# Kernel optimization log

Hardware: AMD Instinct MI355X
Metric: run time of the kernel (lower is better)

## Reference

```python
import jax, jax.numpy as jnp
import numpy as np

N_NODES = 50000
N_EDGES = 500000
NODE_DIM = 128
EDGE_DIM = 128
HIDDEN = 256


def setup_inputs() -> dict:
    key = jax.random.key(0)
    k1, k2, k3, k4, k5 = jax.random.split(key, 5)
    node_features = jax.random.normal(k1, (N_NODES, NODE_DIM), dtype=jnp.float32)
    edge_features = jax.random.normal(k2, (N_EDGES, EDGE_DIM), dtype=jnp.float32)
    edge_index = jax.random.randint(k3, (2, N_EDGES), 0, N_NODES, dtype=jnp.int64)
    in_dim = 2 * NODE_DIM + EDGE_DIM
    W1 = jax.random.normal(k4, (in_dim, HIDDEN), dtype=jnp.float32) * (1.0 / np.sqrt(in_dim))
    b1 = jnp.zeros((HIDDEN,), dtype=jnp.float32)
    W2 = jax.random.normal(k5, (HIDDEN, EDGE_DIM), dtype=jnp.float32) * (1.0 / np.sqrt(HIDDEN))
    b2 = jnp.zeros((EDGE_DIM,), dtype=jnp.float32)
    return {"node_features": node_features, "edge_features": edge_features,
            "edge_index": edge_index, "W1": W1, "b1": b1, "W2": W2, "b2": b2}


def reference(node_features, edge_features, edge_index, W1, b1, W2, b2):
    # h_edge' = h_edge + MLP(concat(h_src, h_dst, h_edge)); dropout is identity (eval)
    src, dst = edge_index[0], edge_index[1]
    h_src = node_features[src]                    # (E, node_dim)
    h_dst = node_features[dst]                    # (E, node_dim)
    combined = jnp.concatenate([h_src, h_dst, edge_features], axis=1)  # (E, 2*nd+ed)
    h = jax.nn.relu(combined @ W1 + b1)           # (E, hidden)
    update = h @ W2 + b2                          # (E, edge_dim)
    return edge_features + update
```

## Files before the change

kernel.cpp:

```cpp
#include <hip/hip_runtime.h>

#define E_TOTAL   500000
#define NN        50000
#define ND        128
#define ED        128
#define HID       256
#define IND       384
#define EB        64
#define NBLOCKS   ((E_TOTAL + EB - 1) / EB)

typedef float  f32x4  __attribute__((ext_vector_type(4)));
typedef short  bf16x8 __attribute__((ext_vector_type(8)));

__device__ __forceinline__ unsigned short f2bf(float f) {
    unsigned int u = __float_as_uint(f);
    u += 0x7FFFu + ((u >> 16) & 1u);
    return (unsigned short)(u >> 16);
}
__device__ __forceinline__ float bf2f(unsigned short h) {
    return __uint_as_float(((unsigned int)h) << 16);
}

__global__ void prep_w1(const float* __restrict__ w1, unsigned short* __restrict__ w1t) {
    int i = blockIdx.x * blockDim.x + threadIdx.x;
    if (i >= IND * HID) return;
    int k = i / HID, n = i % HID;
    w1t[n * IND + k] = f2bf(w1[i]);
}

__global__ void prep_w2(const float* __restrict__ w2, unsigned short* __restrict__ w2t) {
    int i = blockIdx.x * blockDim.x + threadIdx.x;
    if (i >= HID * ED) return;
    int k = i / ED, n = i % ED;
    w2t[n * HID + k] = f2bf(w2[i]);
}

__global__ __launch_bounds__(256, 2)
void prep_ptab(const float* __restrict__ nf,
               const unsigned short* __restrict__ w1t,
               const float* __restrict__ b1,
               unsigned short* __restrict__ Psrc,
               unsigned short* __restrict__ Pdst) {
    __shared__ unsigned short An[EB * ND];
    const int tid  = threadIdx.x;
    const int base = blockIdx.x * EB;
    const int lane = tid & 63;
    const int w    = tid >> 6;
    const int l15  = lane & 15;
    const int lhi  = lane >> 4;

    #pragma unroll
    for (int it = 0; it < 4; ++it) {
        int item = tid + it * 256;
        int row = item >> 4, cc = item & 15;
        int nidx = base + row;
        if (nidx >= NN) nidx = NN - 1;
        const float* p = nf + (size_t)nidx * ND + cc * 8;
        float4 f0 = *(const float4*)p;
        float4 f1 = *(const float4*)(p + 4);
        bf16x8 val;
        val[0] = (short)f2bf(f0.x); val[1] = (short)f2bf(f0.y);
        val[2] = (short)f2bf(f0.z); val[3] = (short)f2bf(f0.w);
        val[4] = (short)f2bf(f1.x); val[5] = (short)f2bf(f1.y);
        val[6] = (short)f2bf(f1.z); val[7] = (short)f2bf(f1.w);
        *(bf16x8*)(An + row * ND + ((cc * 8) ^ ((row & 7) * 8))) = val;
    }
    __syncthreads();

    f32x4 accs[4][4], accd[4][4];
    #pragma unroll
    for (int mt = 0; mt < 4; ++mt)
        #pragma unroll
        for (int nt = 0; nt < 4; ++nt) { accs[mt][nt] = (f32x4)0.0f; accd[mt][nt] = (f32x4)0.0f; }

    #pragma unroll
    for (int ks = 0; ks < 4; ++ks) {
        int c0 = ks * 32 + lhi * 8;
        bf16x8 a[4];
        #pragma unroll
        for (int mt = 0; mt < 4; ++mt) {
            int row = mt * 16 + l15;
            a[mt] = *(const bf16x8*)(An + row * ND + (c0 ^ ((row & 7) * 8)));
        }
        #pragma unroll
        for (int nt = 0; nt < 4; ++nt) {
            int n = w * 64 + nt * 16 + l15;
            bf16x8 bs = *(const bf16x8*)(w1t + (size_t)n * IND + c0);
            bf16x8 bd = *(const bf16x8*)(w1t + (size_t)n * IND + 128 + c0);
            #pragma unroll
            for (int mt = 0; mt < 4; ++mt) {
                accs[mt][nt] = __builtin_amdgcn_mfma_f32_16x16x32_bf16(a[mt], bs, accs[mt][nt], 0, 0, 0);
                accd[mt][nt] = __builtin_amdgcn_mfma_f32_16x16x32_bf16(a[mt], bd, accd[mt][nt], 0, 0, 0);
            }
        }
    }

    #pragma unroll
    for (int nt = 0; nt < 4; ++nt) {
        int col = w * 64 + nt * 16 + l15;
        float bias = b1[col];
        #pragma unroll
        for (int mt = 0; mt < 4; ++mt) {
            #pragma unroll
            for (int r = 0; r < 4; ++r) {
                int row = mt * 16 + lhi * 4 + r;
                int nidx = base + row;
                if (nidx < NN) {
                    size_t off = (size_t)nidx * HID + col;
                    Psrc[off] = f2bf(accs[mt][nt][r] + bias);
                    Pdst[off] = f2bf(accd[mt][nt][r]);
                }
            }
        }
    }
}

__global__ __launch_bounds__(256, 3)
void edge_mlp(const float* __restrict__ edgef,
              const int* __restrict__ eidx,
              const unsigned short* __restrict__ Psrc,
              const unsigned short* __restrict__ Pdst,
              const unsigned short* __restrict__ w1t,
              const unsigned short* __restrict__ w2t,
              const float* __restrict__ b2,
              float* __restrict__ out) {
    __shared__ unsigned short Ae[EB * ND];
    __shared__ unsigned short Hs[EB * HID];

    const int tid  = threadIdx.x;
    const int base = blockIdx.x * EB;
    const int lane = tid & 63;
    const int w    = tid >> 6;
    const int l15  = lane & 15;
    const int lhi  = lane >> 4;
    const int* srcI = eidx;
    const int* dstI = eidx + E_TOTAL;

    #pragma unroll
    for (int it = 0; it < 4; ++it) {
        int item = tid + it * 256;
        int row = item >> 4, cc = item & 15;
        int e = base + row;
        int el = e < E_TOTAL ? e : E_TOTAL - 1;
        const float* p = edgef + (size_t)el * ED + cc * 8;
        float4 f0 = *(const float4*)p;
        float4 f1 = *(const float4*)(p + 4);
        bf16x8 val;
        val[0] = (short)f2bf(f0.x); val[1] = (short)f2bf(f0.y);
        val[2] = (short)f2bf(f0.z); val[3] = (short)f2bf(f0.w);
        val[4] = (short)f2bf(f1.x); val[5] = (short)f2bf(f1.y);
        val[6] = (short)f2bf(f1.z); val[7] = (short)f2bf(f1.w);
        *(bf16x8*)(Ae + row * ND + ((cc * 8) ^ ((row & 7) * 8))) = val;
    }

    #pragma unroll
    for (int it = 0; it < 8; ++it) {
        int item = tid + it * 256;
        int row = item >> 5, cc = item & 31;
        int e = base + row;
        int el = e < E_TOTAL ? e : E_TOTAL - 1;
        int s = srcI[el], d = dstI[el];
        bf16x8 vs = *(const bf16x8*)(Psrc + (size_t)s * HID + cc * 8);
        bf16x8 vd = *(const bf16x8*)(Pdst + (size_t)d * HID + cc * 8);
        bf16x8 o;
        #pragma unroll
        for (int j = 0; j < 8; ++j)
            o[j] = (short)f2bf(bf2f((unsigned short)vs[j]) + bf2f((unsigned short)vd[j]));
        *(bf16x8*)(Hs + row * HID + ((cc * 8) ^ ((row & 7) * 8))) = o;
    }
    __syncthreads();

    f32x4 acc1[4][4];
    #pragma unroll
    for (int mt = 0; mt < 4; ++mt)
        #pragma unroll
        for (int nt = 0; nt < 4; ++nt)
            acc1[mt][nt] = (f32x4)0.0f;

    #pragma unroll
    for (int ks = 0; ks < 4; ++ks) {
        int c0 = ks * 32 + lhi * 8;
        bf16x8 a[4];
        #pragma unroll
        for (int mt = 0; mt < 4; ++mt) {
            int row = mt * 16 + l15;
            a[mt] = *(const bf16x8*)(Ae + row * ND + (c0 ^ ((row & 7) * 8)));
        }
        #pragma unroll
        for (int nt = 0; nt < 4; ++nt) {
            int n = w * 64 + nt * 16 + l15;
            bf16x8 b = *(const bf16x8*)(w1t + (size_t)n * IND + 256 + c0);
            #pragma unroll
            for (int mt = 0; mt < 4; ++mt)
                acc1[mt][nt] = __builtin_amdgcn_mfma_f32_16x16x32_bf16(a[mt], b, acc1[mt][nt], 0, 0, 0);
        }
    }

    #pragma unroll
    for (int nt = 0; nt < 4; ++nt) {
        int col = w * 64 + nt * 16 + l15;
        #pragma unroll
        for (int mt = 0; mt < 4; ++mt) {
            #pragma unroll
            for (int r = 0; r < 4; ++r) {
                int row = mt * 16 + lhi * 4 + r;
                int idx = row * HID + (col ^ ((row & 7) * 8));
                float v = acc1[mt][nt][r] + bf2f(Hs[idx]);
                v = v > 0.0f ? v : 0.0f;
                Hs[idx] = f2bf(v);
            }
        }
    }
    __syncthreads();

    f32x4 acc2[4][2];
    #pragma unroll
    for (int mt = 0; mt < 4; ++mt)
        #pragma unroll
        for (int nt = 0; nt < 2; ++nt)
            acc2[mt][nt] = (f32x4)0.0f;

    #pragma unroll
    for (int ks = 0; ks < 8; ++ks) {
        int c0 = ks * 32 + lhi * 8;
        bf16x8 a[4];
        #pragma unroll
        for (int mt = 0; mt < 4; ++mt) {
            int row = mt * 16 + l15;
            a[mt] = *(const bf16x8*)(Hs + row * HID + (c0 ^ ((row & 7) * 8)));
        }
        #pragma unroll
        for (int nt = 0; nt < 2; ++nt) {
            int n = w * 32 + nt * 16 + l15;
            bf16x8 b = *(const bf16x8*)(w2t + (size_t)n * HID + c0);
            #pragma unroll
            for (int mt = 0; mt < 4; ++mt)
                acc2[mt][nt] = __builtin_amdgcn_mfma_f32_16x16x32_bf16(a[mt], b, acc2[mt][nt], 0, 0, 0);
        }
    }

    #pragma unroll
    for (int nt = 0; nt < 2; ++nt) {
        int col = w * 32 + nt * 16 + l15;
        float bias = b2[col];
        #pragma unroll
        for (int mt = 0; mt < 4; ++mt) {
            #pragma unroll
            for (int r = 0; r < 4; ++r) {
                int row = mt * 16 + lhi * 4 + r;
                int e = base + row;
                if (e < E_TOTAL) {
                    float ev = bf2f(Ae[row * ND + (col ^ ((row & 7) * 8))]);
                    out[(size_t)e * ED + col] = ev + acc2[mt][nt][r] + bias;
                }
            }
        }
    }
}

extern "C" void kernel_launch(void* const* d_in, const int* in_sizes, int n_in,
                              void* d_out, int out_size, void* d_ws, size_t ws_size,
                              hipStream_t stream) {
    const float* nf   = (const float*)d_in[0];
    const float* ef   = (const float*)d_in[1];
    const int*   eidx = (const int*)d_in[2];
    const float* W1   = (const float*)d_in[3];
    const float* b1   = (const float*)d_in[4];
    const float* W2   = (const float*)d_in[5];
    const float* b2   = (const float*)d_in[6];
    float* out = (float*)d_out;

    unsigned short* w1t  = (unsigned short*)d_ws;
    unsigned short* w2t  = w1t + IND * HID;
    unsigned short* Psrc = w2t + HID * ED;
    unsigned short* Pdst = Psrc + (size_t)NN * HID;

    prep_w1<<<(IND * HID + 255) / 256, 256, 0, stream>>>(W1, w1t);
    prep_w2<<<(HID * ED + 255) / 256, 256, 0, stream>>>(W2, w2t);
    prep_ptab<<<(NN + EB - 1) / EB, 256, 0, stream>>>(nf, w1t, b1, Psrc, Pdst);
    edge_mlp<<<NBLOCKS, 256, 0, stream>>>(ef, eidx, Psrc, Pdst, w1t, w2t, b2, out);
}
```

Baseline: 289.6 us.

## Gather node projections asynchronously into LDS and overlap with first GEMM

The per-edge gather of the precomputed src/dst node projections now uses global_load_lds directly into two separate LDS buffers. These loads are issued before the edge-feature conversion and the edge GEMM and waited on only after it, so gather latency can overlap with MFMA work. The W1 edge-slice fragments are preloaded into registers and the indices are loaded up front. The trade-off is doubled LDS for P buffers and more registers, so launch bounds drop to 2 blocks per SM. The sum of the two projections now happens in fp32 during the ReLU epilogue.

```diff
diff --git a/kernel.cpp b/kernel.cpp
--- a/kernel.cpp
+++ b/kernel.cpp
@@ -115,7 +115,7 @@
     }
 }
 
-__global__ __launch_bounds__(256, 3)
+__global__ __launch_bounds__(256, 2)
 void edge_mlp(const float* __restrict__ edgef,
               const int* __restrict__ eidx,
               const unsigned short* __restrict__ Psrc,
@@ -125,7 +125,8 @@
               const float* __restrict__ b2,
               float* __restrict__ out) {
     __shared__ unsigned short Ae[EB * ND];
-    __shared__ unsigned short Hs[EB * HID];
+    __shared__ unsigned short Ps[EB * HID];
+    __shared__ unsigned short Pd[EB * HID];
 
     const int tid  = threadIdx.x;
     const int base = blockIdx.x * EB;
@@ -133,9 +134,31 @@
     const int w    = tid >> 6;
     const int l15  = lane & 15;
     const int lhi  = lane >> 4;
+    const int rsub = lane >> 5;
+    const int cc32 = lane & 31;
     const int* srcI = eidx;
     const int* dstI = eidx + E_TOTAL;
 
+    int sI[8], dI[8];
+    #pragma unroll
+    for (int i = 0; i < 8; ++i) {
+        int row = w * 16 + 2 * i + rsub;
+        int e = base + row;
+        int el = e < E_TOTAL ? e : E_TOTAL - 1;
+        sI[i] = srcI[el];
+        dI[i] = dstI[el];
+    }
+
+    bf16x8 bfr[4][4];
+    #pragma unroll
+    for (int nt = 0; nt < 4; ++nt) {
+        int n = w * 64 + nt * 16 + l15;
+        #pragma unroll
+        for (int ks = 0; ks < 4; ++ks)
+            bfr[nt][ks] = *(const bf16x8*)(w1t + (size_t)n * IND + 256 + ks * 32 + lhi * 8);
+    }
+
+    float4 ae0[4], ae1[4];
     #pragma unroll
     for (int it = 0; it < 4; ++it) {
         int item = tid + it * 256;
@@ -143,32 +166,43 @@
         int e = base + row;
         int el = e < E_TOTAL ? e : E_TOTAL - 1;
         const float* p = edgef + (size_t)el * ED + cc * 8;
-        float4 f0 = *(const float4*)p;
-        float4 f1 = *(const float4*)(p + 4);
+        ae0[it] = *(const float4*)p;
+        ae1[it] = *(const float4*)(p + 4);
+    }
+
+    __builtin_amdgcn_sched_barrier(0);
+
+    #pragma unroll
+    for (int i = 0; i < 8; ++i) {
+        int row = w * 16 + 2 * i + rsub;
+        int ccs = cc32 ^ (row & 7);
+        const unsigned short* gs = Psrc + (size_t)sI[i] * HID + ccs * 8;
+        const unsigned short* gd = Pdst + (size_t)dI[i] * HID + ccs * 8;
+        unsigned short* ls = Ps + (w * 16 + 2 * i) * HID;
+        unsigned short* ld_ = Pd + (w * 16 + 2 * i) * HID;
+        __builtin_amdgcn_global_load_lds(
+            (const __attribute__((address_space(1))) unsigned int*)gs,
+            (__attribute__((address_space(3))) unsigned int*)ls, 16, 0, 0);
+        __builtin_amdgcn_global_load_lds(
+            (const __attribute__((address_space(1))) unsigned int*)gd,
+            (__attribute__((address_space(3))) unsigned int*)ld_, 16, 0, 0);
+    }
+
+    __builtin_amdgcn_sched_barrier(0);
+
+    #pragma unroll
+    for (int it = 0; it < 4; ++it) {
+        int item = tid + it * 256;
+        int row = item >> 4, cc = item & 15;
         bf16x8 val;
-        val[0] = (short)f2bf(f0.x); val[1] = (short)f2bf(f0.y);
-        val[2] = (short)f2bf(f0.z); val[3] = (short)f2bf(f0.w);
-        val[4] = (short)f2bf(f1.x); val[5] = (short)f2bf(f1.y);
-        val[6] = (short)f2bf(f1.z); val[7] = (short)f2bf(f1.w);
+        val[0] = (short)f2bf(ae0[it].x); val[1] = (short)f2bf(ae0[it].y);
+        val[2] = (short)f2bf(ae0[it].z); val[3] = (short)f2bf(ae0[it].w);
+        val[4] = (short)f2bf(ae1[it].x); val[5] = (short)f2bf(ae1[it].y);
+        val[6] = (short)f2bf(ae1[it].z); val[7] = (short)f2bf(ae1[it].w);
         *(bf16x8*)(Ae + row * ND + ((cc * 8) ^ ((row & 7) * 8))) = val;
     }
-
-    #pragma unroll
-    for (int it = 0; it < 8; ++it) {
-        int item = tid + it * 256;
-        int row = item >> 5, cc = item & 31;
-        int e = base + row;
-        int el = e < E_TOTAL ? e : E_TOTAL - 1;
-        int s = srcI[el], d = dstI[el];
-        bf16x8 vs = *(const bf16x8*)(Psrc + (size_t)s * HID + cc * 8);
-        bf16x8 vd = *(const bf16x8*)(Pdst + (size_t)d * HID + cc * 8);
-        bf16x8 o;
-        #pragma unroll
-        for (int j = 0; j < 8; ++j)
-            o[j] = (short)f2bf(bf2f((unsigned short)vs[j]) + bf2f((unsigned short)vd[j]));
-        *(bf16x8*)(Hs + row * HID + ((cc * 8) ^ ((row & 7) * 8))) = o;
-    }
-    __syncthreads();
+    asm volatile("s_waitcnt lgkmcnt(0)" ::: "memory");
+    __builtin_amdgcn_s_barrier();
 
     f32x4 acc1[4][4];
     #pragma unroll
@@ -187,14 +221,15 @@
             a[mt] = *(const bf16x8*)(Ae + row * ND + (c0 ^ ((row & 7) * 8)));
         }
         #pragma unroll
-        for (int nt = 0; nt < 4; ++nt) {
-            int n = w * 64 + nt * 16 + l15;
-            bf16x8 b = *(const bf16x8*)(w1t + (size_t)n * IND + 256 + c0);
+        for (int nt = 0; nt < 4; ++nt)
             #pragma unroll
             for (int mt = 0; mt < 4; ++mt)
-                acc1[mt][nt] = __builtin_amdgcn_mfma_f32_16x16x32_bf16(a[mt], b, acc1[mt][nt], 0, 0, 0);
-        }
-    }
+                acc1[mt][nt] = __builtin_amdgcn_mfma_f32_16x16x32_bf16(a[mt], bfr[nt][ks], acc1[mt][nt], 0, 0, 0);
+    }
+
+    __builtin_amdgcn_sched_barrier(0);
+    asm volatile("s_waitcnt vmcnt(0) lgkmcnt(0)" ::: "memory");
+    __builtin_amdgcn_s_barrier();
 
     #pragma unroll
     for (int nt = 0; nt < 4; ++nt) {
@@ -205,13 +240,14 @@
             for (int r = 0; r < 4; ++r) {
                 int row = mt * 16 + lhi * 4 + r;
                 int idx = row * HID + (col ^ ((row & 7) * 8));
-                float v = acc1[mt][nt][r] + bf2f(Hs[idx]);
+                float v = acc1[mt][nt][r] + bf2f(Ps[idx]) + bf2f(Pd[idx]);
                 v = v > 0.0f ? v : 0.0f;
-                Hs[idx] = f2bf(v);
+                Ps[idx] = f2bf(v);
             }
         }
     }
-    __syncthreads();
+    asm volatile("s_waitcnt lgkmcnt(0)" ::: "memory");
+    __builtin_amdgcn_s_barrier();
 
     f32x4 acc2[4][2];
     #pragma unroll
@@ -227,7 +263,7 @@
         #pragma unroll
         for (int mt = 0; mt < 4; ++mt) {
             int row = mt * 16 + l15;
-            a[mt] = *(const bf16x8*)(Hs + row * HID + (c0 ^ ((row & 7) * 8)));
+            a[mt] = *(const bf16x8*)(Ps + row * HID + (c0 ^ ((row & 7) * 8)));
         }
         #pragma unroll
         for (int nt = 0; nt < 2; ++nt) {
```

New measurement: 366.2 us. 26.4% more time.

## Load edge features directly into MFMA registers, drop the Ae LDS buffer

Applied to the files above, without the earlier changes.

Removes the shared-memory staging buffer for edge features. Each wave now loads its A fragments for the first GEMM straight from global memory and converts them to bf16 in registers, and the residual add re-reads edge features from global memory in fp32 rather than the bf16 LDS copy. The first sync now sits after the first GEMM. Freeing 16KB of LDS per block lets occupancy rise, and launch bounds go from 3 to 5 blocks. The cost is redundant global reads of edge features across the four waves, uncoalesced row-strided fragment loads, and more register pressure under the tighter bound.

```diff
diff --git a/kernel.cpp b/kernel.cpp
--- a/kernel.cpp
+++ b/kernel.cpp
@@ -115,7 +115,7 @@
     }
 }
 
-__global__ __launch_bounds__(256, 3)
+__global__ __launch_bounds__(256, 5)
 void edge_mlp(const float* __restrict__ edgef,
               const int* __restrict__ eidx,
               const unsigned short* __restrict__ Psrc,
@@ -124,7 +124,6 @@
               const unsigned short* __restrict__ w2t,
               const float* __restrict__ b2,
               float* __restrict__ out) {
-    __shared__ unsigned short Ae[EB * ND];
     __shared__ unsigned short Hs[EB * HID];
 
     const int tid  = threadIdx.x;
@@ -135,23 +134,6 @@
     const int lhi  = lane >> 4;
     const int* srcI = eidx;
     const int* dstI = eidx + E_TOTAL;
-
-    #pragma unroll
-    for (int it = 0; it < 4; ++it) {
-        int item = tid + it * 256;
-        int row = item >> 4, cc = item & 15;
-        int e = base + row;
-        int el = e < E_TOTAL ? e : E_TOTAL - 1;
-        const float* p = edgef + (size_t)el * ED + cc * 8;
-        float4 f0 = *(const float4*)p;
-        float4 f1 = *(const float4*)(p + 4);
-        bf16x8 val;
-        val[0] = (short)f2bf(f0.x); val[1] = (short)f2bf(f0.y);
-        val[2] = (short)f2bf(f0.z); val[3] = (short)f2bf(f0.w);
-        val[4] = (short)f2bf(f1.x); val[5] = (short)f2bf(f1.y);
-        val[6] = (short)f2bf(f1.z); val[7] = (short)f2bf(f1.w);
-        *(bf16x8*)(Ae + row * ND + ((cc * 8) ^ ((row & 7) * 8))) = val;
-    }
 
     #pragma unroll
     for (int it = 0; it < 8; ++it) {
@@ -168,7 +150,14 @@
             o[j] = (short)f2bf(bf2f((unsigned short)vs[j]) + bf2f((unsigned short)vd[j]));
         *(bf16x8*)(Hs + row * HID + ((cc * 8) ^ ((row & 7) * 8))) = o;
     }
-    __syncthreads();
+
+    const float* pA[4];
+    #pragma unroll
+    for (int mt = 0; mt < 4; ++mt) {
+        int e = base + mt * 16 + l15;
+        int el = e < E_TOTAL ? e : E_TOTAL - 1;
+        pA[mt] = edgef + (size_t)el * ED;
+    }
 
     f32x4 acc1[4][4];
     #pragma unroll
@@ -183,8 +172,12 @@
         bf16x8 a[4];
         #pragma unroll
         for (int mt = 0; mt < 4; ++mt) {
-            int row = mt * 16 + l15;
-            a[mt] = *(const bf16x8*)(Ae + row * ND + (c0 ^ ((row & 7) * 8)));
+            float4 f0 = *(const float4*)(pA[mt] + c0);
+            float4 f1 = *(const float4*)(pA[mt] + c0 + 4);
+            a[mt][0] = (short)f2bf(f0.x); a[mt][1] = (short)f2bf(f0.y);
+            a[mt][2] = (short)f2bf(f0.z); a[mt][3] = (short)f2bf(f0.w);
+            a[mt][4] = (short)f2bf(f1.x); a[mt][5] = (short)f2bf(f1.y);
+            a[mt][6] = (short)f2bf(f1.z); a[mt][7] = (short)f2bf(f1.w);
         }
         #pragma unroll
         for (int nt = 0; nt < 4; ++nt) {
@@ -195,6 +188,7 @@
                 acc1[mt][nt] = __builtin_amdgcn_mfma_f32_16x16x32_bf16(a[mt], b, acc1[mt][nt], 0, 0, 0);
         }
     }
+    __syncthreads();
 
     #pragma unroll
     for (int nt = 0; nt < 4; ++nt) {
@@ -250,8 +244,8 @@
                 int row = mt * 16 + lhi * 4 + r;
                 int e = base + row;
                 if (e < E_TOTAL) {
-                    float ev = bf2f(Ae[row * ND + (col ^ ((row & 7) * 8))]);
-                    out[(size_t)e * ED + col] = ev + acc2[mt][nt][r] + bias;
+                    size_t off = (size_t)e * ED + col;
+                    out[off] = edgef[off] + acc2[mt][nt][r] + bias;
                 }
             }
         }
```

Measured after the change: 679.8 us. +134.7%, slower.

## Split edge MLP across eight waves per block and merge weight prep kernels

Applied to the files above, without the earlier changes.

The edge_mlp block grows from 256 to 512 threads. Each wave now computes half as many output columns in both GEMMs, which cuts accumulator registers and puts more resident waves on each CU to hide the latency of the random node-table gathers. The gather of the precomputed node tables is moved ahead of the edge-feature load so the long-latency loads are issued first. The two weight-prep kernels are fused into one launch. The cost is that each wave reloads the same A fragments from LDS, doubling total LDS read traffic, plus more barrier participants per block.

```diff
diff --git a/kernel.cpp b/kernel.cpp
--- a/kernel.cpp
+++ b/kernel.cpp
@@ -21,18 +21,17 @@
     return __uint_as_float(((unsigned int)h) << 16);
 }
 
-__global__ void prep_w1(const float* __restrict__ w1, unsigned short* __restrict__ w1t) {
+__global__ void prep_weights(const float* __restrict__ w1, const float* __restrict__ w2,
+                             unsigned short* __restrict__ w1t, unsigned short* __restrict__ w2t) {
     int i = blockIdx.x * blockDim.x + threadIdx.x;
-    if (i >= IND * HID) return;
-    int k = i / HID, n = i % HID;
-    w1t[n * IND + k] = f2bf(w1[i]);
-}
-
-__global__ void prep_w2(const float* __restrict__ w2, unsigned short* __restrict__ w2t) {
-    int i = blockIdx.x * blockDim.x + threadIdx.x;
-    if (i >= HID * ED) return;
-    int k = i / ED, n = i % ED;
-    w2t[n * HID + k] = f2bf(w2[i]);
+    if (i < IND * HID) {
+        int k = i / HID, n = i % HID;
+        w1t[n * IND + k] = f2bf(w1[i]);
+    } else if (i < IND * HID + HID * ED) {
+        int q = i - IND * HID;
+        int k = q / ED, n = q % ED;
+        w2t[n * HID + k] = f2bf(w2[q]);
+    }
 }
 
 __global__ __launch_bounds__(256, 2)
@@ -41,9 +40,9 @@
                const float* __restrict__ b1,
                unsigned short* __restrict__ Psrc,
                unsigned short* __restrict__ Pdst) {
-    __shared__ unsigned short An[EB * ND];
+    __shared__ unsigned short An[64 * ND];
     const int tid  = threadIdx.x;
-    const int base = blockIdx.x * EB;
+    const int base = blockIdx.x * 64;
     const int lane = tid & 63;
     const int w    = tid >> 6;
     const int l15  = lane & 15;
@@ -115,7 +114,7 @@
     }
 }
 
-__global__ __launch_bounds__(256, 3)
+__global__ __launch_bounds__(512, 6)
 void edge_mlp(const float* __restrict__ edgef,
               const int* __restrict__ eidx,
               const unsigned short* __restrict__ Psrc,
@@ -138,7 +137,23 @@
 
     #pragma unroll
     for (int it = 0; it < 4; ++it) {
-        int item = tid + it * 256;
+        int item = tid + it * 512;
+        int row = item >> 5, cc = item & 31;
+        int e = base + row;
+        int el = e < E_TOTAL ? e : E_TOTAL - 1;
+        int s = srcI[el], d = dstI[el];
+        bf16x8 vs = *(const bf16x8*)(Psrc + (size_t)s * HID + cc * 8);
+        bf16x8 vd = *(const bf16x8*)(Pdst + (size_t)d * HID + cc * 8);
+        bf16x8 o;
+        #pragma unroll
+        for (int j = 0; j < 8; ++j)
+            o[j] = (short)f2bf(bf2f((unsigned short)vs[j]) + bf2f((unsigned short)vd[j]));
+        *(bf16x8*)(Hs + row * HID + ((cc * 8) ^ ((row & 7) * 8))) = o;
+    }
+
+    #pragma unroll
+    for (int it = 0; it < 2; ++it) {
+        int item = tid + it * 512;
         int row = item >> 4, cc = item & 15;
         int e = base + row;
         int el = e < E_TOTAL ? e : E_TOTAL - 1;
@@ -152,29 +167,13 @@
         val[6] = (short)f2bf(f1.z); val[7] = (short)f2bf(f1.w);
         *(bf16x8*)(Ae + row * ND + ((cc * 8) ^ ((row & 7) * 8))) = val;
     }
-
-    #pragma unroll
-    for (int it = 0; it < 8; ++it) {
-        int item = tid + it * 256;
-        int row = item >> 5, cc = item & 31;
-        int e = base + row;
-        int el = e < E_TOTAL ? e : E_TOTAL - 1;
-        int s = srcI[el], d = dstI[el];
-        bf16x8 vs = *(const bf16x8*)(Psrc + (size_t)s * HID + cc * 8);
-        bf16x8 vd = *(const bf16x8*)(Pdst + (size_t)d * HID + cc * 8);
-        bf16x8 o;
-        #pragma unroll
-        for (int j = 0; j < 8; ++j)
-            o[j] = (short)f2bf(bf2f((unsigned short)vs[j]) + bf2f((unsigned short)vd[j]));
-        *(bf16x8*)(Hs + row * HID + ((cc * 8) ^ ((row & 7) * 8))) = o;
-    }
     __syncthreads();
 
-    f32x4 acc1[4][4];
+    f32x4 acc1[4][2];
     #pragma unroll
     for (int mt = 0; mt < 4; ++mt)
         #pragma unroll
-        for (int nt = 0; nt < 4; ++nt)
+        for (int nt = 0; nt < 2; ++nt)
             acc1[mt][nt] = (f32x4)0.0f;
 
     #pragma unroll
@@ -187,8 +186,8 @@
             a[mt] = *(const bf16x8*)(Ae + row * ND + (c0 ^ ((row & 7) * 8)));
         }
         #pragma unroll
-        for (int nt = 0; nt < 4; ++nt) {
-            int n = w * 64 + nt * 16 + l15;
+        for (int nt = 0; nt < 2; ++nt) {
+            int n = w * 32 + nt * 16 + l15;
             bf16x8 b = *(const bf16x8*)(w1t + (size_t)n * IND + 256 + c0);
             #pragma unroll
             for (int mt = 0; mt < 4; ++mt)
@@ -197,8 +196,8 @@
     }
 
     #pragma unroll
-    for (int nt = 0; nt < 4; ++nt) {
-        int col = w * 64 + nt * 16 + l15;
+    for (int nt = 0; nt < 2; ++nt) {
+        int col = w * 32 + nt * 16 + l15;
         #pragma unroll
         for (int mt = 0; mt < 4; ++mt) {
             #pragma unroll
@@ -213,12 +212,9 @@
     }
     __syncthreads();
 
-    f32x4 acc2[4][2];
-    #pragma unroll
-    for (int mt = 0; mt < 4; ++mt)
-        #pragma unroll
-        for (int nt = 0; nt < 2; ++nt)
-            acc2[mt][nt] = (f32x4)0.0f;
+    f32x4 acc2[4];
+    #pragma unroll
+    for (int mt = 0; mt < 4; ++mt) acc2[mt] = (f32x4)0.0f;
 
     #pragma unroll
     for (int ks = 0; ks < 8; ++ks) {
@@ -229,19 +225,15 @@
             int row = mt * 16 + l15;
             a[mt] = *(const bf16x8*)(Hs + row * HID + (c0 ^ ((row & 7) * 8)));
         }
-        #pragma unroll
-        for (int nt = 0; nt < 2; ++nt) {
-            int n = w * 32 + nt * 16 + l15;
-            bf16x8 b = *(const bf16x8*)(w2t + (size_t)n * HID + c0);
-            #pragma unroll
-            for (int mt = 0; mt < 4; ++mt)
-                acc2[mt][nt] = __builtin_amdgcn_mfma_f32_16x16x32_bf16(a[mt], b, acc2[mt][nt], 0, 0, 0);
-        }
-    }
-
-    #pragma unroll
-    for (int nt = 0; nt < 2; ++nt) {
-        int col = w * 32 + nt * 16 + l15;
+        int n = w * 16 + l15;
+        bf16x8 b = *(const bf16x8*)(w2t + (size_t)n * HID + c0);
+        #pragma unroll
+        for (int mt = 0; mt < 4; ++mt)
+            acc2[mt] = __builtin_amdgcn_mfma_f32_16x16x32_bf16(a[mt], b, acc2[mt], 0, 0, 0);
+    }
+
+    {
+        int col = w * 16 + l15;
         float bias = b2[col];
         #pragma unroll
         for (int mt = 0; mt < 4; ++mt) {
@@ -251,7 +243,7 @@
                 int e = base + row;
                 if (e < E_TOTAL) {
                     float ev = bf2f(Ae[row * ND + (col ^ ((row & 7) * 8))]);
-                    out[(size_t)e * ED + col] = ev + acc2[mt][nt][r] + bias;
+                    out[(size_t)e * ED + col] = ev + acc2[mt][r] + bias;
                 }
             }
         }
@@ -275,8 +267,8 @@
     unsigned short* Psrc = w2t + HID * ED;
     unsigned short* Pdst = Psrc + (size_t)NN * HID;
 
-    prep_w1<<<(IND * HID + 255) / 256, 256, 0, stream>>>(W1, w1t);
-    prep_w2<<<(HID * ED + 255) / 256, 256, 0, stream>>>(W2, w2t);
-    prep_ptab<<<(NN + EB - 1) / EB, 256, 0, stream>>>(nf, w1t, b1, Psrc, Pdst);
-    edge_mlp<<<NBLOCKS, 256, 0, stream>>>(ef, eidx, Psrc, Pdst, w1t, w2t, b2, out);
-}
+    int wtotal = IND * HID + HID * ED;
+    prep_weights<<<(wtotal + 255) / 256, 256, 0, stream>>>(W1, W2, w1t, w2t);
+    prep_ptab<<<(NN + 63) / 64, 256, 0, stream>>>(nf, w1t, b1, Psrc, Pdst);
+    edge_mlp<<<NBLOCKS, 512, 0, stream>>>(ef, eidx, Psrc, Pdst, w1t, w2t, b2, out);
+}
```

Result: slower. 326.2 us (+12.6%).
